# Kernel tuning notes

Hardware: AMD Instinct MI355X
Metric: run time of the kernel (lower is better)

Reference implementation:

```python
import jax, jax.numpy as jnp
import numpy as np
import math

B, T, D = 2, 2048, 1024
H = 16
d = D // H
I = 2816
RMS_EPS = 1e-6
GN_EPS = 1e-5


def setup_inputs() -> dict:
    key = jax.random.key(0)
    ks = jax.random.split(key, 12)
    s = 0.02
    gammas = 1.0 - jnp.exp(jnp.linspace(math.log(0.1), math.log(0.001), H)).astype(jnp.float32)
    return {
        "x": jax.random.normal(ks[0], (B, T, D), dtype=jnp.float32),
        "ln1_w": jnp.ones((D,), jnp.float32),
        "ln2_w": jnp.ones((D,), jnp.float32),
        "Wq": jax.random.normal(ks[1], (D, D), jnp.float32) * s,
        "Wk": jax.random.normal(ks[2], (D, D), jnp.float32) * s,
        "Wv": jax.random.normal(ks[3], (D, D), jnp.float32) * s,
        "Wg": jax.random.normal(ks[4], (D, D), jnp.float32) * s,
        "Wo": jax.random.normal(ks[5], (D, D), jnp.float32) * s,
        "gamma": gammas,
        "gn_w": jnp.ones((D,), jnp.float32),
        "gn_b": jnp.zeros((D,), jnp.float32),
        "gate_w": jax.random.normal(ks[6], (I, D), jnp.float32) * s,
        "up_w": jax.random.normal(ks[7], (I, D), jnp.float32) * s,
        "down_w": jax.random.normal(ks[8], (D, I), jnp.float32) * s,
    }


def _rmsnorm(x, w):
    var = jnp.mean(x * x, axis=-1, keepdims=True)
    return (x * jax.lax.rsqrt(var + RMS_EPS)) * w


def _retnet_scan(q, k, v, gamma):
    # q,k,v: (B,T,H,d); gamma: (H,)
    qT = jnp.moveaxis(q, 1, 0)  # (T,B,H,d)
    kT = jnp.moveaxis(k, 1, 0)
    vT = jnp.moveaxis(v, 1, 0)

    def step(S, qkv_t):
        q_t, k_t, v_t = qkv_t
        # S: (B,H,d,d) ; outer product k_t v_t^T
        S = gamma[None, :, None, None] * S + k_t[..., :, None] * v_t[..., None, :]
        o_t = jnp.einsum('bhd,bhde->bhe', q_t, S)
        return S, o_t

    S0 = jnp.zeros((q.shape[0], H, d, d), q.dtype)
    _, yT = jax.lax.scan(step, S0, (qT, kT, vT))  # yT: (T,B,H,d)
    return jnp.moveaxis(yT, 0, 1)  # (B,T,H,d)


def _group_norm(y, gn_w, gn_b):
    # y: (B,T,H,d). torch GroupNorm(H groups) on (B,D,T): normalize per (b, head)
    # over the (T, d) extent.
    mean = jnp.mean(y, axis=(1, 3), keepdims=True)
    var = jnp.var(y, axis=(1, 3), keepdims=True)
    yn = (y - mean) * jax.lax.rsqrt(var + GN_EPS)
    return yn * gn_w.reshape(1, 1, H, d) + gn_b.reshape(1, 1, H, d)


def reference(x, ln1_w, ln2_w, Wq, Wk, Wv, Wg, Wo, gamma, gn_w, gn_b, gate_w, up_w, down_w):
    Bx, Tx, Dx = x.shape
    h = _rmsnorm(x, ln1_w)
    q = (h @ Wq.T).reshape(Bx, Tx, H, d)
    k = (h @ Wk.T).reshape(Bx, Tx, H, d)
    v = (h @ Wv.T).reshape(Bx, Tx, H, d)
    g = jax.nn.sigmoid(h @ Wg.T)
    gam = jax.nn.sigmoid(gamma)
    y = _retnet_scan(q, k, v, gam)          # (B,T,H,d)
    y = _group_norm(y, gn_w, gn_b).reshape(Bx, Tx, Dx)
    y = g * y
    x = x + y @ Wo.T
    h2 = _rmsnorm(x, ln2_w)
    mlp = (jax.nn.silu(h2 @ gate_w.T) * (h2 @ up_w.T)) @ down_w.T
    return x + mlp
```

## Files before the change

### kernel.cpp

```cpp
#include <hip/hip_runtime.h>
#include <hip/hip_bf16.h>
#include <cstdint>
#include <cstddef>

typedef __bf16 bf16_t;
typedef __bf16 bf16x4 __attribute__((ext_vector_type(4)));
typedef __bf16 bf16x8 __attribute__((ext_vector_type(8)));
typedef float f32x4 __attribute__((ext_vector_type(4)));

#define DEVINL __device__ __forceinline__

#define TT 2048
#define DD 1024
#define HH 16
#define II 2816

DEVINL float waveSum(float v) {
#pragma unroll
  for (int m = 32; m >= 1; m >>= 1) v += __shfl_xor(v, m, 64);
  return v;
}

DEVINL float sigmoidf_(float z) { return 1.0f / (1.0f + __expf(-z)); }

DEVINL void gload_lds16(const bf16_t* g, bf16_t* l) {
  __builtin_amdgcn_global_load_lds((const __attribute__((address_space(1))) void*)g,
                                   (__attribute__((address_space(3))) void*)l, 16, 0, 0);
}

__global__ __launch_bounds__(256) void prep_kernel(const float* __restrict__ Wq,
                                                   const float* __restrict__ Wk,
                                                   const float* __restrict__ Wv,
                                                   const float* __restrict__ Wg,
                                                   const float* __restrict__ Wo,
                                                   const float* __restrict__ gate_w,
                                                   const float* __restrict__ up_w,
                                                   const float* __restrict__ down_w,
                                                   bf16_t* __restrict__ Wqkvg_bf,
                                                   bf16_t* __restrict__ Wo_bf,
                                                   bf16_t* __restrict__ GU_bf,
                                                   bf16_t* __restrict__ down_bf,
                                                   float* __restrict__ stats) {
  const int bid = blockIdx.x;
  const int tid = threadIdx.x;
  if (bid == 0 && tid < 64) stats[tid] = 0.f;
  if (bid < 5120) {
    const int which = bid >> 10;
    const float* src;
    bf16_t* dst;
    switch (which) {
      case 0: src = Wq; dst = Wqkvg_bf; break;
      case 1: src = Wk; dst = Wqkvg_bf + (size_t)DD * DD; break;
      case 2: src = Wv; dst = Wqkvg_bf + 2 * (size_t)DD * DD; break;
      case 3: src = Wg; dst = Wqkvg_bf + 3 * (size_t)DD * DD; break;
      default: src = Wo; dst = Wo_bf; break;
    }
    const int i = (bid & 1023) * 256 + tid;
    float4 v = reinterpret_cast<const float4*>(src)[i];
    bf16x4 o;
    o[0] = (bf16_t)v.x; o[1] = (bf16_t)v.y; o[2] = (bf16_t)v.z; o[3] = (bf16_t)v.w;
    reinterpret_cast<bf16x4*>(dst)[i] = o;
  } else if (bid < 10752) {
    const int r = bid - 5120;
    const int jb = r >> 5, s = r & 31;
    const float* src = (s < 16) ? (gate_w + (size_t)(jb * 16 + s) * DD)
                                : (up_w + (size_t)(jb * 16 + s - 16) * DD);
    float4 v = reinterpret_cast<const float4*>(src)[tid];
    bf16x4 o;
    o[0] = (bf16_t)v.x; o[1] = (bf16_t)v.y; o[2] = (bf16_t)v.z; o[3] = (bf16_t)v.w;
    reinterpret_cast<bf16x4*>(GU_bf + (size_t)r * DD)[tid] = o;
  } else {
    const int i = (bid - 10752) * 256 + tid;
    float4 v = reinterpret_cast<const float4*>(down_w)[i];
    bf16x4 o;
    o[0] = (bf16_t)v.x; o[1] = (bf16_t)v.y; o[2] = (bf16_t)v.z; o[3] = (bf16_t)v.w;
    reinterpret_cast<bf16x4*>(down_bf)[i] = o;
  }
}

__global__ __launch_bounds__(256) void rmsnorm_kernel(const float* __restrict__ x,
                                                      const float* __restrict__ w,
                                                      bf16_t* __restrict__ out) {
  const int row = blockIdx.x;
  const int tid = threadIdx.x;
  const float4 v = reinterpret_cast<const float4*>(x + (size_t)row * DD)[tid];
  float ss = v.x * v.x + v.y * v.y + v.z * v.z + v.w * v.w;
  ss = waveSum(ss);
  __shared__ float red[4];
  if ((tid & 63) == 0) red[tid >> 6] = ss;
  __syncthreads();
  const float total = red[0] + red[1] + red[2] + red[3];
  const float rstd = rsqrtf(total * (1.0f / (float)DD) + 1e-6f);
  const float4 wv = reinterpret_cast<const float4*>(w)[tid];
  bf16x4 o;
  o[0] = (bf16_t)(v.x * rstd * wv.x);
  o[1] = (bf16_t)(v.y * rstd * wv.y);
  o[2] = (bf16_t)(v.z * rstd * wv.z);
  o[3] = (bf16_t)(v.w * rstd * wv.w);
  reinterpret_cast<bf16x4*>(out + (size_t)row * DD)[tid] = o;
}

template <int EPI>
__global__ __launch_bounds__(512, 4) void gemm128x256(const bf16_t* __restrict__ A,
                                                      const bf16_t* __restrict__ B,
                                                      bf16_t* __restrict__ O1,
                                                      bf16_t* __restrict__ O2,
                                                      int M, int N, int K) {
  extern __shared__ __align__(16) char lds[];
  const int tid = threadIdx.x;
  const int wid = tid >> 6;
  const int lane = tid & 63;
  const int wr = wid >> 2;
  const int wc = wid & 3;

  const int gx = gridDim.x;
  const int nwg = gx * gridDim.y;
  int flat = blockIdx.y * gx + blockIdx.x;
  flat = (flat & 7) * (nwg >> 3) + (flat >> 3);
  const int row0 = (flat / gx) * 128;
  const int col0 = (flat % gx) * 256;

  const int ls_row = lane >> 2;
  const int ls_col = ((lane & 3) ^ ((lane >> 3) & 3)) * 8;
  const bf16_t* gA = A + (size_t)(row0 + wid * 16 + ls_row) * K + ls_col;
  const bf16_t* gB = B + (size_t)(col0 + wid * 32 + ls_row) * K + ls_col;

  const int kq = lane >> 4;
  const int rl = lane & 15;
  const int xg = (rl >> 1) & 3;
  const int gsel = (kq ^ xg) << 4;

  f32x4 acc[4][4] = {};
  const int nt = K >> 5;

  auto stage = [&](int t) {
    char* slot = lds + (t % 3) * 24576;
    const int ko = t << 5;
    gload_lds16(gA + ko, (bf16_t*)(slot + wid * 1024));
#pragma unroll
    for (int j = 0; j < 2; ++j)
      gload_lds16(gB + (size_t)j * 16 * K + ko,
                  (bf16_t*)(slot + 8192 + wid * 2048 + j * 1024));
  };

  stage(0); stage(1);
  asm volatile("s_waitcnt vmcnt(3)" ::: "memory");
  __builtin_amdgcn_s_barrier();
  __builtin_amdgcn_sched_barrier(0);

  for (int t = 0; t < nt; ++t) {
    if (t + 2 < nt) stage(t + 2);
    const char* ab = lds + (t % 3) * 24576;
    const char* bb = ab + 8192;
    bf16x8 aF[4], bF[4];
#pragma unroll
    for (int n = 0; n < 4; ++n)
      bF[n] = *reinterpret_cast<const bf16x8*>(bb + (wc * 64 + n * 16 + rl) * 64 + gsel);
#pragma unroll
    for (int m = 0; m < 4; ++m)
      aF[m] = *reinterpret_cast<const bf16x8*>(ab + (wr * 64 + m * 16 + rl) * 64 + gsel);
    __builtin_amdgcn_s_setprio(1);
#pragma unroll
    for (int m = 0; m < 4; ++m)
#pragma unroll
      for (int n = 0; n < 4; ++n)
        acc[m][n] = __builtin_amdgcn_mfma_f32_16x16x32_bf16(aF[m], bF[n], acc[m][n], 0, 0, 0);
    __builtin_amdgcn_s_setprio(0);
    if (t + 2 < nt) {
      asm volatile("s_waitcnt vmcnt(3)" ::: "memory");
    } else if (t + 2 == nt) {
      asm volatile("s_waitcnt vmcnt(0)" ::: "memory");
    }
    __builtin_amdgcn_s_barrier();
    __builtin_amdgcn_sched_barrier(0);
  }

  const int crow = row0 + wr * 64 + kq * 4;
  const int ccol = col0 + wc * 64 + rl;
  if (EPI == 2) {
    const int obase = (col0 + wc * 64) / 2 + rl;
#pragma unroll
    for (int m = 0; m < 4; ++m)
#pragma unroll
      for (int p = 0; p < 2; ++p)
#pragma unroll
        for (int r = 0; r < 4; ++r) {
          const float g = acc[m][2 * p][r];
          const float u = acc[m][2 * p + 1][r];
          O1[(size_t)(crow + m * 16 + r) * II + (obase + p * 16)] =
              (bf16_t)(g * sigmoidf_(g) * u);
        }
  } else {
    if (col0 < 3072) {
#pragma unroll
      for (int m = 0; m < 4; ++m)
#pragma unroll
        for (int n = 0; n < 4; ++n)
#pragma unroll
          for (int r = 0; r < 4; ++r)
            O1[(size_t)(crow + m * 16 + r) * 3072 + (ccol + n * 16)] = (bf16_t)acc[m][n][r];
    } else {
#pragma unroll
      for (int m = 0; m < 4; ++m)
#pragma unroll
        for (int n = 0; n < 4; ++n)
#pragma unroll
          for (int r = 0; r < 4; ++r)
            O2[(size_t)(crow + m * 16 + r) * DD + (ccol + n * 16 - 3072)] =
                (bf16_t)sigmoidf_(acc[m][n][r]);
    }
  }
}

template <int EPI>
__global__ __launch_bounds__(256) void gemm_bt(const bf16_t* __restrict__ A,
                                               const bf16_t* __restrict__ B,
                                               float* __restrict__ C,
                                               const float* __restrict__ addsrc,
                                               int M, int N, int K) {
  __shared__ __align__(16) bf16_t smA[128 * 32];
  __shared__ __align__(16) bf16_t smB[128 * 32];
  const int tid = threadIdx.x;
  const int wid = tid >> 6;
  const int lane = tid & 63;
  const int row0 = blockIdx.y * 128;
  const int col0 = blockIdx.x * 128;
  const int wr = wid >> 1, wc = wid & 1;

  f32x4 acc[4][4] = {};

  const int sr = (wid * 2) * 16 + (lane >> 2);
  const int sc = (((lane & 3) ^ ((lane >> 3) & 3))) * 8;
  const bf16_t* gA = A + (size_t)(row0 + sr) * K + sc;
  const bf16_t* gB = B + (size_t)(col0 + sr) * K + sc;
  bf16_t* lA = smA + wid * 1024;
  bf16_t* lB = smB + wid * 1024;

  const int rl = lane & 15;
  const int kq = lane >> 4;
  const int xg = (rl >> 1) & 3;
  const int ge = (kq ^ xg) * 8;
  const int aoff = (wr * 64 + rl) * 32 + ge;
  const int boff = (wc * 64 + rl) * 32 + ge;

  for (int k0 = 0; k0 < K; k0 += 32) {
#pragma unroll
    for (int j2 = 0; j2 < 2; ++j2) {
      gload_lds16(gA + (size_t)j2 * 16 * K + k0, lA + j2 * 512);
      gload_lds16(gB + (size_t)j2 * 16 * K + k0, lB + j2 * 512);
    }
    __syncthreads();
    bf16x8 aF[4], bF[4];
#pragma unroll
    for (int m = 0; m < 4; ++m)
      aF[m] = *reinterpret_cast<const bf16x8*>(smA + aoff + m * 16 * 32);
#pragma unroll
    for (int n = 0; n < 4; ++n)
      bF[n] = *reinterpret_cast<const bf16x8*>(smB + boff + n * 16 * 32);
#pragma unroll
    for (int m = 0; m < 4; ++m)
#pragma unroll
      for (int n = 0; n < 4; ++n)
        acc[m][n] = __builtin_amdgcn_mfma_f32_16x16x32_bf16(aF[m], bF[n], acc[m][n], 0, 0, 0);
    __syncthreads();
  }

  const int crow = row0 + wr * 64 + kq * 4;
  const int ccol = col0 + wc * 64 + rl;
#pragma unroll
  for (int m = 0; m < 4; ++m)
#pragma unroll
    for (int n = 0; n < 4; ++n)
#pragma unroll
      for (int r = 0; r < 4; ++r) {
        const size_t idx = (size_t)(crow + m * 16 + r) * N + (ccol + n * 16);
        float v = acc[m][n][r];
        if (EPI == 1) v += addsrc[idx];
        C[idx] = v;
      }
}

__global__ __launch_bounds__(256) void retscan_mfma(const bf16_t* __restrict__ qkv,
                                                    const float* __restrict__ gamma,
                                                    float* __restrict__ y,
                                                    float* __restrict__ stats) {
  const int c = blockIdx.x;
  const int bh = blockIdx.y;
  const int b = bh >> 4;
  const int h = bh & 15;
  const int tid = threadIdx.x;
  const int w = tid >> 6;
  const int lane = tid & 63;
  const int kq = lane >> 4;
  const int rl = lane & 15;

  __shared__ __align__(16) bf16_t K_lds[128 * 64];
  __shared__ __align__(16) bf16_t VT_lds[64 * 128];
  __shared__ __align__(16) bf16_t P_lds[64 * 128];
  __shared__ float rs[4][2];

  const size_t rstr = 3 * DD;
  const bf16_t* base = qkv + (size_t)(b * TT) * rstr + h * 64;
  const bf16_t* kgl = base + DD;
  const bf16_t* vgl = base + 2 * DD;

  for (int g = tid; g < 1024; g += 256) {
    const int sw = g >> 3, gr = g & 7;
    const int t = c * 64 - 64 + sw;
    bf16x8 kv = {};
    bf16x8 vv = {};
    if (t >= 0) {
      kv = *reinterpret_cast<const bf16x8*>(kgl + (size_t)t * rstr + gr * 8);
      vv = *reinterpret_cast<const bf16x8*>(vgl + (size_t)t * rstr + gr * 8);
    }
    *reinterpret_cast<bf16x8*>(K_lds + sw * 64 + ((gr ^ (sw & 7)) << 3)) = kv;
#pragma unroll
    for (int j = 0; j < 8; ++j) {
      const int e = gr * 8 + j;
      const int gs = (sw >> 3) ^ (e & 7);
      VT_lds[e * 128 + (gs << 3) + (sw & 7)] = vv[j];
    }
  }

  const int i0 = w * 16;
  const bf16_t* qrow = base + (size_t)(c * 64 + i0 + rl) * rstr;
  bf16x8 qF0 = *reinterpret_cast<const bf16x8*>(qrow + kq * 8);
  bf16x8 qF1 = *reinterpret_cast<const bf16x8*>(qrow + 32 + kq * 8);
  const float gam = sigmoidf_(gamma[h]);
  const float l2g = __log2f(gam);
  const float gi16 = exp2f(-16.f * l2g);

  __syncthreads();

  f32x4 S[8];
#pragma unroll
  for (int st = 0; st < 8; ++st) {
    const int sw = st * 16 + rl;
    const bf16_t* krow = K_lds + sw * 64;
    bf16x8 kF0 = *reinterpret_cast<const bf16x8*>(krow + ((kq ^ (sw & 7)) << 3));
    bf16x8 kF1 = *reinterpret_cast<const bf16x8*>(krow + (((4 + kq) ^ (sw & 7)) << 3));
    f32x4 s = {};
    s = __builtin_amdgcn_mfma_f32_16x16x32_bf16(qF0, kF0, s, 0, 0, 0);
    s = __builtin_amdgcn_mfma_f32_16x16x32_bf16(qF1, kF1, s, 0, 0, 0);
    S[st] = s;
  }

  float wgt[4];
  int lag[4];
#pragma unroll
  for (int r = 0; r < 4; ++r) {
    lag[r] = 64 + i0 + kq * 4 + r - rl;
    wgt[r] = exp2f((float)lag[r] * l2g);
  }
#pragma unroll
  for (int st = 0; st < 8; ++st) {
    const int sw = st * 16 + rl;
#pragma unroll
    for (int r = 0; r < 4; ++r) {
      const float p = (lag[r] >= 0) ? S[st][r] * wgt[r] : 0.f;
      const int i = i0 + kq * 4 + r;
      const int gs = (sw >> 3) ^ (i & 7);
      P_lds[i * 128 + (gs << 3) + (sw & 7)] = (bf16_t)p;
      lag[r] -= 16;
      wgt[r] *= gi16;
    }
  }
  asm volatile("s_waitcnt lgkmcnt(0)" ::: "memory");
  __builtin_amdgcn_sched_barrier(0);

  f32x4 Y[4] = {};
#pragma unroll
  for (int ks = 0; ks < 4; ++ks) {
    const int ia = i0 + rl;
    const int ga = (ks * 4 + kq) ^ (ia & 7);
    bf16x8 aF = *reinterpret_cast<const bf16x8*>(P_lds + ia * 128 + (ga << 3));
#pragma unroll
    for (int et = 0; et < 4; ++et) {
      const int e = et * 16 + rl;
      const int gb = (ks * 4 + kq) ^ (e & 7);
      bf16x8 bF = *reinterpret_cast<const bf16x8*>(VT_lds + e * 128 + (gb << 3));
      Y[et] = __builtin_amdgcn_mfma_f32_16x16x32_bf16(aF, bF, Y[et], 0, 0, 0);
    }
  }

  float s = 0.f, ss = 0.f;
  const size_t ybase = (size_t)(b * TT + c * 64 + i0 + kq * 4) * DD + h * 64 + rl;
#pragma unroll
  for (int et = 0; et < 4; ++et)
#pragma unroll
    for (int r = 0; r < 4; ++r) {
      const float v = Y[et][r];
      s += v;
      ss += v * v;
      y[ybase + (size_t)r * DD + et * 16] = v;
    }
  s = waveSum(s);
  ss = waveSum(ss);
  if (lane == 0) { rs[w][0] = s; rs[w][1] = ss; }
  __syncthreads();
  if (tid == 0) {
    atomicAdd(&stats[bh * 2], rs[0][0] + rs[1][0] + rs[2][0] + rs[3][0]);
    atomicAdd(&stats[bh * 2 + 1], rs[0][1] + rs[1][1] + rs[2][1] + rs[3][1]);
  }
}

__global__ __launch_bounds__(256) void gn_apply_kernel(const float* __restrict__ y,
                                                       const float* __restrict__ stats,
                                                       const bf16_t* __restrict__ gsig,
                                                       const float* __restrict__ gn_w,
                                                       const float* __restrict__ gn_b,
                                                       bf16_t* __restrict__ out) {
  const int row = blockIdx.x;
  const int tid = threadIdx.x;
  const int col = tid * 4;
  const int b = row >> 11;
  const int h = col >> 6;
  const float S = stats[(b * HH + h) * 2];
  const float SS = stats[(b * HH + h) * 2 + 1];
  const float inv = 1.0f / ((float)TT * 64.0f);
  const float mean = S * inv;
  const float var = SS * inv - mean * mean;
  const float rstd = rsqrtf(var + 1e-5f);
  float4 v = reinterpret_cast<const float4*>(y + (size_t)row * DD)[tid];
  float4 wv = reinterpret_cast<const float4*>(gn_w)[tid];
  float4 bv = reinterpret_cast<const float4*>(gn_b)[tid];
  bf16x4 gv = reinterpret_cast<const bf16x4*>(gsig + (size_t)row * DD)[tid];
  bf16x4 o;
  o[0] = (bf16_t)((((v.x - mean) * rstd) * wv.x + bv.x) * (float)gv[0]);
  o[1] = (bf16_t)((((v.y - mean) * rstd) * wv.y + bv.y) * (float)gv[1]);
  o[2] = (bf16_t)((((v.z - mean) * rstd) * wv.z + bv.z) * (float)gv[2]);
  o[3] = (bf16_t)((((v.w - mean) * rstd) * wv.w + bv.w) * (float)gv[3]);
  reinterpret_cast<bf16x4*>(out + (size_t)row * DD)[tid] = o;
}

extern "C" void kernel_launch(void* const* d_in, const int* in_sizes, int n_in,
                              void* d_out, int out_size, void* d_ws, size_t ws_size,
                              hipStream_t stream) {
  const float* x = (const float*)d_in[0];
  const float* ln1_w = (const float*)d_in[1];
  const float* ln2_w = (const float*)d_in[2];
  const float* Wq = (const float*)d_in[3];
  const float* Wk = (const float*)d_in[4];
  const float* Wv = (const float*)d_in[5];
  const float* Wg = (const float*)d_in[6];
  const float* Wo = (const float*)d_in[7];
  const float* gamma = (const float*)d_in[8];
  const float* gn_w = (const float*)d_in[9];
  const float* gn_b = (const float*)d_in[10];
  const float* gate_w = (const float*)d_in[11];
  const float* up_w = (const float*)d_in[12];
  const float* down_w = (const float*)d_in[13];
  float* out = (float*)d_out;

  const int M = 2 * TT;

  char* ws = (char*)d_ws;
  size_t off = 0;
  auto alloc = [&](size_t bytes) -> void* {
    void* p = ws + off;
    off += (bytes + 255) & ~(size_t)255;
    return p;
  };
  bf16_t* h_bf = (bf16_t*)alloc((size_t)M * DD * 2);
  bf16_t* Wqkvg_bf = (bf16_t*)alloc((size_t)4 * DD * DD * 2);
  bf16_t* Wo_bf = (bf16_t*)alloc((size_t)DD * DD * 2);
  bf16_t* GU_bf = (bf16_t*)alloc((size_t)2 * II * DD * 2);
  bf16_t* down_bf = (bf16_t*)alloc((size_t)DD * II * 2);
  bf16_t* qkv_bf = (bf16_t*)alloc((size_t)M * 3 * DD * 2);
  bf16_t* gsig = (bf16_t*)alloc((size_t)M * DD * 2);
  float* yBuf = (float*)alloc((size_t)M * DD * 4);
  bf16_t* ygated = (bf16_t*)alloc((size_t)M * DD * 2);
  bf16_t* act = (bf16_t*)alloc((size_t)M * II * 2);
  float* stats = (float*)alloc(64 * 4);
  (void)ws_size; (void)in_sizes; (void)n_in; (void)out_size;

  float* x2 = yBuf;

  prep_kernel<<<13568, 256, 0, stream>>>(Wq, Wk, Wv, Wg, Wo, gate_w, up_w, down_w,
                                         Wqkvg_bf, Wo_bf, GU_bf, down_bf, stats);

  rmsnorm_kernel<<<M, 256, 0, stream>>>(x, ln1_w, h_bf);

  {
    dim3 g(4 * DD / 256, M / 128);
    gemm128x256<3><<<g, 512, 73728, stream>>>(h_bf, Wqkvg_bf, qkv_bf, gsig, M, 4 * DD, DD);
  }

  {
    dim3 g(TT / 64, 2 * HH);
    retscan_mfma<<<g, 256, 0, stream>>>(qkv_bf, gamma, yBuf, stats);
  }

  gn_apply_kernel<<<M, 256, 0, stream>>>(yBuf, stats, gsig, gn_w, gn_b, ygated);

  {
    dim3 g(DD / 128, M / 128);
    gemm_bt<1><<<g, 256, 0, stream>>>(ygated, Wo_bf, x2, x, M, DD, DD);
  }

  rmsnorm_kernel<<<M, 256, 0, stream>>>(x2, ln2_w, h_bf);

  {
    dim3 g(2 * II / 256, M / 128);
    gemm128x256<2><<<g, 512, 73728, stream>>>(h_bf, GU_bf, act, nullptr, M, 2 * II, DD);
  }

  {
    dim3 g(DD / 128, M / 128);
    gemm_bt<1><<<g, 256, 0, stream>>>(act, down_bf, out, x2, M, DD, II);
  }
}
```

Measured before the change: 251.6 us.

## Split-K the Wo and down projections with atomic accumulation

Replaces the residual-add GEMMs with a split-K variant that spreads K across four grid slices and accumulates into the output with float atomicAdd. The residual is copied into the output buffer first by a new copy kernel. The intent is to fill the GPU, since the original 8x32 grid of 256 blocks underuses the CUs. The cost is two extra copy kernels, atomic traffic on fp32 outputs, and a summation order that is no longer deterministic.

Result: slower. 313.0 us (+24.4%).

```diff
diff --git a/kernel.cpp b/kernel.cpp
--- a/kernel.cpp
+++ b/kernel.cpp
@@ -78,6 +78,12 @@
   }
 }
 
+__global__ __launch_bounds__(256) void copy_f32_kernel(const float* __restrict__ src,
+                                                       float* __restrict__ dst, int n4) {
+  for (int i = blockIdx.x * 256 + threadIdx.x; i < n4; i += gridDim.x * 256)
+    reinterpret_cast<float4*>(dst)[i] = reinterpret_cast<const float4*>(src)[i];
+}
+
 __global__ __launch_bounds__(256) void rmsnorm_kernel(const float* __restrict__ x,
                                                       const float* __restrict__ w,
                                                       bf16_t* __restrict__ out) {
@@ -212,12 +218,10 @@
   }
 }
 
-template <int EPI>
-__global__ __launch_bounds__(256) void gemm_bt(const bf16_t* __restrict__ A,
-                                               const bf16_t* __restrict__ B,
-                                               float* __restrict__ C,
-                                               const float* __restrict__ addsrc,
-                                               int M, int N, int K) {
+__global__ __launch_bounds__(256) void gemm_bt_sk(const bf16_t* __restrict__ A,
+                                                  const bf16_t* __restrict__ B,
+                                                  float* __restrict__ C,
+                                                  int M, int N, int K, int Ksub) {
   __shared__ __align__(16) bf16_t smA[128 * 32];
   __shared__ __align__(16) bf16_t smB[128 * 32];
   const int tid = threadIdx.x;
@@ -225,14 +229,15 @@
   const int lane = tid & 63;
   const int row0 = blockIdx.y * 128;
   const int col0 = blockIdx.x * 128;
+  const int kbase = blockIdx.z * Ksub;
   const int wr = wid >> 1, wc = wid & 1;
 
   f32x4 acc[4][4] = {};
 
   const int sr = (wid * 2) * 16 + (lane >> 2);
   const int sc = (((lane & 3) ^ ((lane >> 3) & 3))) * 8;
-  const bf16_t* gA = A + (size_t)(row0 + sr) * K + sc;
-  const bf16_t* gB = B + (size_t)(col0 + sr) * K + sc;
+  const bf16_t* gA = A + (size_t)(row0 + sr) * K + kbase + sc;
+  const bf16_t* gB = B + (size_t)(col0 + sr) * K + kbase + sc;
   bf16_t* lA = smA + wid * 1024;
   bf16_t* lB = smB + wid * 1024;
 
@@ -243,7 +248,7 @@
   const int aoff = (wr * 64 + rl) * 32 + ge;
   const int boff = (wc * 64 + rl) * 32 + ge;
 
-  for (int k0 = 0; k0 < K; k0 += 32) {
+  for (int k0 = 0; k0 < Ksub; k0 += 32) {
 #pragma unroll
     for (int j2 = 0; j2 < 2; ++j2) {
       gload_lds16(gA + (size_t)j2 * 16 * K + k0, lA + j2 * 512);
@@ -274,9 +279,7 @@
 #pragma unroll
       for (int r = 0; r < 4; ++r) {
         const size_t idx = (size_t)(crow + m * 16 + r) * N + (ccol + n * 16);
-        float v = acc[m][n][r];
-        if (EPI == 1) v += addsrc[idx];
-        C[idx] = v;
+        atomicAdd(&C[idx], acc[m][n][r]);
       }
 }
 
@@ -475,6 +478,7 @@
   (void)ws_size; (void)in_sizes; (void)n_in; (void)out_size;
 
   float* x2 = yBuf;
+  const int n4_MD = M * DD / 4;
 
   prep_kernel<<<13568, 256, 0, stream>>>(Wq, Wk, Wv, Wg, Wo, gate_w, up_w, down_w,
                                          Wqkvg_bf, Wo_bf, GU_bf, down_bf, stats);
@@ -493,9 +497,10 @@
 
   gn_apply_kernel<<<M, 256, 0, stream>>>(yBuf, stats, gsig, gn_w, gn_b, ygated);
 
+  copy_f32_kernel<<<2048, 256, 0, stream>>>(x, x2, n4_MD);
   {
-    dim3 g(DD / 128, M / 128);
-    gemm_bt<1><<<g, 256, 0, stream>>>(ygated, Wo_bf, x2, x, M, DD, DD);
+    dim3 g(DD / 128, M / 128, 4);
+    gemm_bt_sk<<<g, 256, 0, stream>>>(ygated, Wo_bf, x2, M, DD, DD, DD / 4);
   }
 
   rmsnorm_kernel<<<M, 256, 0, stream>>>(x2, ln2_w, h_bf);
@@ -505,8 +510,9 @@
     gemm128x256<2><<<g, 512, 73728, stream>>>(h_bf, GU_bf, act, nullptr, M, 2 * II, DD);
   }
 
+  copy_f32_kernel<<<2048, 256, 0, stream>>>(x2, out, n4_MD);
   {
-    dim3 g(DD / 128, M / 128);
-    gemm_bt<1><<<g, 256, 0, stream>>>(act, down_bf, out, x2, M, DD, II);
-  }
-}
+    dim3 g(DD / 128, M / 128, 4);
+    gemm_bt_sk<<<g, 256, 0, stream>>>(act, down_bf, out, M, DD, II, II / 4);
+  }
+}
```
